# Kernel optimization log

Measured on AMD Instinct MI355X. Metric: run time of the kernel, lower is better.

## Reference

```python
import jax, jax.numpy as jnp
import numpy as np

B, N, E, H = 4, 8192, 256, 8
EXP = 4  # params['num_layers'] -> MLP expansion
HID = EXP * E
EPS = 1e-5


def _layernorm(x, w, b):
    mu = jnp.mean(x, axis=-1, keepdims=True)
    var = jnp.mean(jnp.square(x - mu), axis=-1, keepdims=True)
    return (x - mu) * jax.lax.rsqrt(var + EPS) * w + b


def _mish(x):
    return x * jnp.tanh(jax.nn.softplus(x))


def setup_inputs() -> dict:
    key = jax.random.key(0)
    ks = jax.random.split(key, 12)
    s = 0.02
    return {
        "x": jax.random.normal(ks[0], (B, N, E), dtype=jnp.float32),
        "ln1_w": jnp.ones((E,), jnp.float32),
        "ln1_b": jnp.zeros((E,), jnp.float32),
        "Wq": jax.random.normal(ks[1], (E, E), jnp.float32) * s,
        "bq": jnp.zeros((E,), jnp.float32),
        "Wk": jax.random.normal(ks[2], (E, E), jnp.float32) * s,
        "bk": jnp.zeros((E,), jnp.float32),
        "Wv": jax.random.normal(ks[3], (E, E), jnp.float32) * s,
        "bv": jnp.zeros((E,), jnp.float32),
        "Wp": jax.random.normal(ks[4], (E, E), jnp.float32) * s,
        "bp": jnp.zeros((E,), jnp.float32),
        "ln2_w": jnp.ones((E,), jnp.float32),
        "ln2_b": jnp.zeros((E,), jnp.float32),
        "W1": jax.random.normal(ks[5], (HID, E), jnp.float32) * s,
        "b1": jnp.zeros((HID,), jnp.float32),
        "W2": jax.random.normal(ks[6], (E, HID), jnp.float32) * s,
        "b2": jnp.zeros((E,), jnp.float32),
    }


def _msa(x, Wq, bq, Wk, bk, Wv, bv, Wp, bp):
    b, n, e = x.shape
    d = n // H  # sequence-chunk per head (faithful to source rearrange)
    q = (x @ Wq.T + bq).reshape(b, H, d, e)
    k = (x @ Wk.T + bk).reshape(b, H, d, e)
    v = (x @ Wv.T + bv).reshape(b, H, d, e)
    scale = jnp.sqrt(jnp.float32(E))
    energy = jnp.einsum('bhie,bhke->bhik', q, k)  # (b,H,d,d)
    att = jax.nn.softmax(energy, axis=3) / scale
    o = jnp.einsum('bhik,bhke->bhie', att, v).reshape(b, n, e)
    return o @ Wp.T + bp


def reference(x, ln1_w, ln1_b, Wq, bq, Wk, bk, Wv, bv, Wp, bp,
              ln2_w, ln2_b, W1, b1, W2, b2):
    # pre-LN attention block + residual
    x1 = _msa(_layernorm(x, ln1_w, ln1_b), Wq, bq, Wk, bk, Wv, bv, Wp, bp) + x
    # pre-LN MLP (Mish after both linears, per source) + residual
    h = _layernorm(x1, ln2_w, ln2_b)
    h = _mish(h @ W1.T + b1)
    h = _mish(h @ W2.T + b2)
    return h + x1
```

## Files before the change

kernel.cpp:

```cpp
#include <hip/hip_runtime.h>

typedef float  f32x4  __attribute__((ext_vector_type(4)));
typedef float  f4v    __attribute__((ext_vector_type(4)));
typedef __bf16 bf16x8 __attribute__((ext_vector_type(8)));
typedef __bf16 bf16x4 __attribute__((ext_vector_type(4)));
typedef unsigned short ushort_t;

#define AS1 __attribute__((address_space(1)))
#define AS3 __attribute__((address_space(3)))

static __device__ __forceinline__ void gload_lds16(const void* g, void* l) {
  __builtin_amdgcn_global_load_lds((const AS1 void*)g, (AS3 void*)l, 16, 0, 0);
}

static __device__ __forceinline__ float mishf(float x) {
  float t = __expf(x);
  float u = t * (t + 2.f);
  float y = x * __fdividef(u, u + 2.f);
  return (x > 15.f) ? x : y;
}

__global__ __launch_bounds__(256) void castw(
    const float* __restrict__ Wq, const float* __restrict__ Wk,
    const float* __restrict__ Wv, const float* __restrict__ Wp,
    const float* __restrict__ W1, const float* __restrict__ W2,
    __bf16* __restrict__ out)
{
  const int i = (blockIdx.x * 256 + threadIdx.x) * 4;
  const float* src; int off = i;
  if      (i < 65536)  { src = Wq; }
  else if (i < 131072) { src = Wk; off = i - 65536; }
  else if (i < 196608) { src = Wv; off = i - 131072; }
  else if (i < 262144) { src = Wp; off = i - 196608; }
  else if (i < 524288) { src = W1; off = i - 262144; }
  else                 { src = W2; off = i - 524288; }
  const f4v v = *(const f4v*)(src + off);
  bf16x4 o;
  #pragma unroll
  for (int j = 0; j < 4; ++j) o[j] = (__bf16)v[j];
  *(bf16x4*)(out + i) = o;
}

__global__ void packb(const float* __restrict__ a, const float* __restrict__ b,
                      const float* __restrict__ c, float* __restrict__ o) {
  int i = threadIdx.x;
  o[i] = (i < 256) ? a[i] : (i < 512 ? b[i - 256] : c[i - 512]);
}

__global__ __launch_bounds__(256) void ln_rows(
    const float* __restrict__ X, const float* __restrict__ g,
    const float* __restrict__ b, __bf16* __restrict__ Y)
{
  const int l = threadIdx.x & 63;
  const size_t row = (size_t)blockIdx.x * 4 + (threadIdx.x >> 6);
  const f4v x = *(const f4v*)(X + row * 256 + l * 4);
  float s = x[0] + x[1] + x[2] + x[3];
  float q = x[0]*x[0] + x[1]*x[1] + x[2]*x[2] + x[3]*x[3];
  #pragma unroll
  for (int d = 1; d < 64; d <<= 1) { s += __shfl_xor(s, d); q += __shfl_xor(q, d); }
  const float mu = s * (1.f / 256.f);
  const float rs = rsqrtf(q * (1.f / 256.f) - mu * mu + 1e-5f);
  const f4v gv = *(const f4v*)(g + l * 4);
  const f4v bv = *(const f4v*)(b + l * 4);
  bf16x4 o;
  #pragma unroll
  for (int j = 0; j < 4; ++j) o[j] = (__bf16)((x[j] - mu) * rs * gv[j] + bv[j]);
  *(bf16x4*)(Y + row * 256 + l * 4) = o;
}

template<int NT, int KC, int ACT, int RES, int OUTBF>
__global__ __launch_bounds__(512, 2) void bgemm(
    const __bf16* __restrict__ A, const __bf16* __restrict__ Wg,
    const float* __restrict__ bias, const float* __restrict__ res,
    void* __restrict__ out, int ldo)
{
  constexpr int K  = KC * 256;
  constexpr int NB = (KC > 1) ? 2 : 1;
  __shared__ __bf16 Ab[NB][128 * 256];
  const int tid = threadIdx.x, l = tid & 63, w = tid >> 6;
  constexpr int nwg = NT * 256;
  const int wg = (blockIdx.x & 7) * (nwg / 8) + (blockIdx.x >> 3);
  const int mt = wg / NT, nt = wg % NT;
  const int row0 = mt * 128;
  const int col0 = nt * 256 + w * 32;

  auto stageA = [&](int b, int c) {
    #pragma unroll
    for (int j = 0; j < 8; ++j) {
      const int s = j * 512 + tid;
      const int r = s >> 5, q = s & 31;
      gload_lds16(A + (size_t)(row0 + r) * K + c * 256 + ((q ^ (r & 7)) << 3),
                  &Ab[b][s << 3]);
    }
  };

  bf16x8 bf[2][8];
  auto loadB = [&](int c) {
    #pragma unroll
    for (int n = 0; n < 2; ++n)
      #pragma unroll
      for (int u = 0; u < 8; ++u)
        bf[n][u] = *(const bf16x8*)(Wg + (size_t)(col0 + n * 16 + (l & 15)) * K
                                      + c * 256 + u * 32 + ((l >> 4) << 3));
  };

  f32x4 acc[8][2] = {};

  loadB(0);
  stageA(0, 0);
  asm volatile("s_waitcnt vmcnt(0)" ::: "memory");
  __builtin_amdgcn_s_barrier();

  for (int c = 0; c < KC; ++c) {
    const __bf16* La = Ab[c & (NB - 1)];
    if (KC > 1 && c + 1 < KC) stageA((c + 1) & (NB - 1), c + 1);
    #pragma unroll
    for (int u = 0; u < 8; ++u) {
      bf16x8 af[8];
      #pragma unroll
      for (int m = 0; m < 8; ++m) {
        const int r = m * 16 + (l & 15);
        const int q = ((u << 2) | (l >> 4)) ^ (r & 7);
        af[m] = *(const bf16x8*)&La[((r << 5) | q) << 3];
      }
      #pragma unroll
      for (int m = 0; m < 8; ++m) {
        acc[m][0] = __builtin_amdgcn_mfma_f32_16x16x32_bf16(af[m], bf[0][u], acc[m][0], 0, 0, 0);
        acc[m][1] = __builtin_amdgcn_mfma_f32_16x16x32_bf16(af[m], bf[1][u], acc[m][1], 0, 0, 0);
      }
    }
    if (KC > 1 && c + 1 < KC) {
      loadB(c + 1);
      __syncthreads();
    }
  }

  const float b0 = bias[col0 + (l & 15)];
  const float b1 = bias[col0 + 16 + (l & 15)];
  #pragma unroll
  for (int m = 0; m < 8; ++m) {
    #pragma unroll
    for (int r = 0; r < 4; ++r) {
      const int row = row0 + m * 16 + ((l >> 4) << 2) + r;
      float v0 = acc[m][0][r] + b0;
      float v1 = acc[m][1][r] + b1;
      if (ACT) { v0 = mishf(v0); v1 = mishf(v1); }
      if (OUTBF) {
        __bf16* op = (__bf16*)out + (size_t)row * ldo + col0;
        op[l & 15]        = (__bf16)v0;
        op[16 + (l & 15)] = (__bf16)v1;
      } else {
        if (RES) {
          const float* rp = res + (size_t)row * ldo + col0;
          v0 += rp[l & 15];
          v1 += rp[16 + (l & 15)];
        }
        float* op = (float*)out + (size_t)row * ldo + col0;
        op[l & 15]        = v0;
        op[16 + (l & 15)] = v1;
      }
    }
  }
}

__global__ __launch_bounds__(512) void attn_fwd(
    const __bf16* __restrict__ QKV, __bf16* __restrict__ Om)
{
  __shared__ __bf16 Ks[2][32][256];
  __shared__ __bf16 Vs[2][256][32];
  __shared__ __bf16 Ps[8][16][32];
  const int tid = threadIdx.x, l = tid & 63, w = tid >> 6;
  const int wgs = (blockIdx.x & 7) * 32 + (blockIdx.x >> 3);
  const int bh = wgs >> 3, qt = wgs & 7;
  const size_t rbase = (size_t)bh * 1024 * 768;
  const int qr0 = qt * 128 + w * 16;

  bf16x8 qf[8];
  {
    const __bf16* qp = QKV + rbase + (size_t)(qr0 + (l & 15)) * 768 + ((l >> 4) << 3);
    #pragma unroll
    for (int s = 0; s < 8; ++s) qf[s] = *(const bf16x8*)(qp + s * 32);
  }
  f32x4 acc[16] = {};
  float lacc[4] = {0.f, 0.f, 0.f, 0.f};

  const int kec = tid & 31, kr_ = tid >> 5;
  const int vp = tid & 15, vc = tid >> 4;
  const __bf16* gK = QKV + 256 + rbase + kec * 8;
  const __bf16* gV = QKV + 512 + rbase + vc * 8;

  uint4 rk0, rk1, rv0, rv1;
  auto ldKV = [&](int kt) {
    const __bf16* k0 = gK + (size_t)(kt * 32 + kr_) * 768;
    rk0 = *(const uint4*)k0;
    rk1 = *(const uint4*)(k0 + 16 * 768);
    const __bf16* v0 = gV + (size_t)(kt * 32 + vp * 2) * 768;
    rv0 = *(const uint4*)v0;
    rv1 = *(const uint4*)(v0 + 768);
  };
  auto wrKV = [&](int buf) {
    char* kb = (char*)&Ks[buf][0][0];
    const int a0 = (kr_ * 512 + kec * 16) ^ ((kr_ & 15) << 4);
    const int a1 = ((kr_ + 16) * 512 + kec * 16) ^ (((kr_ + 16) & 15) << 4);
    *(uint4*)(kb + a0) = rk0;
    *(uint4*)(kb + a1) = rk1;
    const ushort_t* s0 = (const ushort_t*)&rv0;
    const ushort_t* s1 = (const ushort_t*)&rv1;
    #pragma unroll
    for (int i = 0; i < 8; ++i) {
      unsigned pk = (unsigned)s0[i] | ((unsigned)s1[i] << 16);
      *(unsigned*)&Vs[buf][vc * 8 + i][vp * 2] = pk;
    }
  };

  ldKV(0); wrKV(0);
  __syncthreads();
  int cur = 0;
  for (int kt = 0;;) {
    if (kt + 1 < 32) ldKV(kt + 1);
    f32x4 S[2] = {};
    const char* kbase = (const char*)&Ks[cur][0][0];
    #pragma unroll
    for (int t = 0; t < 2; ++t) {
      const int kcol = t * 16 + (l & 15);
      const int swz = (kcol & 15) << 4;
      #pragma unroll
      for (int s = 0; s < 8; ++s) {
        uint4 kf = *(const uint4*)(kbase + ((kcol * 512 + s * 64 + ((l >> 4) << 4)) ^ swz));
        S[t] = __builtin_amdgcn_mfma_f32_16x16x32_bf16(qf[s], __builtin_bit_cast(bf16x8, kf), S[t], 0, 0, 0);
      }
    }
    #pragma unroll
    for (int t = 0; t < 2; ++t)
      #pragma unroll
      for (int r = 0; r < 4; ++r) {
        float p = __expf(S[t][r]);
        lacc[r] += p;
        Ps[w][((l >> 4) << 2) + r][t * 16 + (l & 15)] = (__bf16)p;
      }
    bf16x8 pf = *(const bf16x8*)&Ps[w][l & 15][(l >> 4) << 3];
    #pragma unroll
    for (int n = 0; n < 16; ++n) {
      uint4 vf = *(const uint4*)&Vs[cur][n * 16 + (l & 15)][(l >> 4) << 3];
      acc[n] = __builtin_amdgcn_mfma_f32_16x16x32_bf16(pf, __builtin_bit_cast(bf16x8, vf), acc[n], 0, 0, 0);
    }
    if (++kt == 32) break;
    wrKV(cur ^ 1);
    __syncthreads();
    cur ^= 1;
  }
  f32x4 inv;
  #pragma unroll
  for (int r = 0; r < 4; ++r) {
    float s = lacc[r];
    s += __shfl_xor(s, 1); s += __shfl_xor(s, 2);
    s += __shfl_xor(s, 4); s += __shfl_xor(s, 8);
    inv[r] = 1.f / (16.f * s);
  }
  __bf16* op = Om + (size_t)(bh * 1024 + qr0 + ((l >> 4) << 2)) * 256 + (l & 15);
  #pragma unroll
  for (int n = 0; n < 16; ++n)
    #pragma unroll
    for (int r = 0; r < 4; ++r)
      op[(size_t)r * 256 + n * 16] = (__bf16)(acc[n][r] * inv[r]);
}

extern "C" void kernel_launch(void* const* d_in, const int* in_sizes, int n_in,
                              void* d_out, int out_size, void* d_ws, size_t ws_size,
                              hipStream_t stream)
{
  const float* x    = (const float*)d_in[0];
  const float* ln1w = (const float*)d_in[1];
  const float* ln1b = (const float*)d_in[2];
  const float* Wq   = (const float*)d_in[3];
  const float* bq   = (const float*)d_in[4];
  const float* Wk   = (const float*)d_in[5];
  const float* bk   = (const float*)d_in[6];
  const float* Wv   = (const float*)d_in[7];
  const float* bv   = (const float*)d_in[8];
  const float* Wp   = (const float*)d_in[9];
  const float* bp   = (const float*)d_in[10];
  const float* ln2w = (const float*)d_in[11];
  const float* ln2b = (const float*)d_in[12];
  const float* W1   = (const float*)d_in[13];
  const float* b1   = (const float*)d_in[14];
  const float* W2   = (const float*)d_in[15];
  const float* b2   = (const float*)d_in[16];

  char* ws = (char*)d_ws;
  __bf16* wb   = (__bf16*)(ws);
  float*  bqkv = (float*)(ws + 1572864);
  __bf16* y    = (__bf16*)(ws + 2097152);
  __bf16* qkv  = (__bf16*)(ws + 18874368);
  float*  x1   = (float*)(ws + 18874368);
  __bf16* hb   = (__bf16*)(ws + 52428800);
  __bf16* h1   = (__bf16*)(ws + 69206016);
  __bf16* ao   = y;
  float*  outp = (float*)d_out;

  castw<<<768, 256, 0, stream>>>(Wq, Wk, Wv, Wp, W1, W2, wb);
  packb<<<1, 768, 0, stream>>>(bq, bk, bv, bqkv);
  ln_rows<<<8192, 256, 0, stream>>>(x, ln1w, ln1b, y);
  bgemm<3, 1, 0, 0, 1><<<768,  512, 0, stream>>>(y,  wb,          bqkv, nullptr, qkv,  768);
  attn_fwd<<<256, 512, 0, stream>>>(qkv, ao);
  bgemm<1, 1, 0, 1, 0><<<256,  512, 0, stream>>>(ao, wb + 196608, bp,   x,       x1,   256);
  ln_rows<<<8192, 256, 0, stream>>>(x1, ln2w, ln2b, hb);
  bgemm<4, 1, 1, 0, 1><<<1024, 512, 0, stream>>>(hb, wb + 262144, b1,   nullptr, h1,  1024);
  bgemm<1, 4, 1, 1, 0><<<256,  512, 0, stream>>>(h1, wb + 524288, b2,   x1,      outp, 256);
}
```

Before: 236.5 us.

## Shrink attention blocks to 256 threads and single-buffer the GEMM A tile

The attention kernel now runs 512 blocks of 256 threads, each handling 64 query rows instead of 128. Each thread loads more K/V per tile, and the V and P shared arrays are padded to 34 columns to avoid bank conflicts. The GEMM drops its double-buffered A tile for a single buffer that is synchronously reloaded per K chunk. This halves LDS use, which should allow more resident blocks, at the cost of no longer overlapping loads with MFMA compute in the K=1024 GEMM.

```diff
diff --git a/kernel.cpp b/kernel.cpp
--- a/kernel.cpp
+++ b/kernel.cpp
@@ -74,9 +74,8 @@
     const float* __restrict__ bias, const float* __restrict__ res,
     void* __restrict__ out, int ldo)
 {
-  constexpr int K  = KC * 256;
-  constexpr int NB = (KC > 1) ? 2 : 1;
-  __shared__ __bf16 Ab[NB][128 * 256];
+  constexpr int K = KC * 256;
+  __shared__ __bf16 Ab[128 * 256];
   const int tid = threadIdx.x, l = tid & 63, w = tid >> 6;
   constexpr int nwg = NT * 256;
   const int wg = (blockIdx.x & 7) * (nwg / 8) + (blockIdx.x >> 3);
@@ -84,13 +83,13 @@
   const int row0 = mt * 128;
   const int col0 = nt * 256 + w * 32;
 
-  auto stageA = [&](int b, int c) {
+  auto stageA = [&](int c) {
     #pragma unroll
     for (int j = 0; j < 8; ++j) {
       const int s = j * 512 + tid;
       const int r = s >> 5, q = s & 31;
       gload_lds16(A + (size_t)(row0 + r) * K + c * 256 + ((q ^ (r & 7)) << 3),
-                  &Ab[b][s << 3]);
+                  &Ab[s << 3]);
     }
   };
 
@@ -106,14 +105,11 @@
 
   f32x4 acc[8][2] = {};
 
-  loadB(0);
-  stageA(0, 0);
+  stageA(0); loadB(0);
   asm volatile("s_waitcnt vmcnt(0)" ::: "memory");
   __builtin_amdgcn_s_barrier();
 
-  for (int c = 0; c < KC; ++c) {
-    const __bf16* La = Ab[c & (NB - 1)];
-    if (KC > 1 && c + 1 < KC) stageA((c + 1) & (NB - 1), c + 1);
+  for (int c = 0;;) {
     #pragma unroll
     for (int u = 0; u < 8; ++u) {
       bf16x8 af[8];
@@ -121,7 +117,7 @@
       for (int m = 0; m < 8; ++m) {
         const int r = m * 16 + (l & 15);
         const int q = ((u << 2) | (l >> 4)) ^ (r & 7);
-        af[m] = *(const bf16x8*)&La[((r << 5) | q) << 3];
+        af[m] = *(const bf16x8*)&Ab[((r << 5) | q) << 3];
       }
       #pragma unroll
       for (int m = 0; m < 8; ++m) {
@@ -129,10 +125,12 @@
         acc[m][1] = __builtin_amdgcn_mfma_f32_16x16x32_bf16(af[m], bf[1][u], acc[m][1], 0, 0, 0);
       }
     }
-    if (KC > 1 && c + 1 < KC) {
-      loadB(c + 1);
-      __syncthreads();
-    }
+    if (++c == KC) break;
+    __syncthreads();
+    stageA(c);
+    loadB(c);
+    asm volatile("s_waitcnt vmcnt(0)" ::: "memory");
+    __builtin_amdgcn_s_barrier();
   }
 
   const float b0 = bias[col0 + (l & 15)];
@@ -163,17 +161,17 @@
   }
 }
 
-__global__ __launch_bounds__(512) void attn_fwd(
+__global__ __launch_bounds__(256) void attn_fwd(
     const __bf16* __restrict__ QKV, __bf16* __restrict__ Om)
 {
   __shared__ __bf16 Ks[2][32][256];
-  __shared__ __bf16 Vs[2][256][32];
-  __shared__ __bf16 Ps[8][16][32];
+  __shared__ __bf16 Vs[2][256][34];
+  __shared__ __bf16 Ps[4][16][34];
   const int tid = threadIdx.x, l = tid & 63, w = tid >> 6;
-  const int wgs = (blockIdx.x & 7) * 32 + (blockIdx.x >> 3);
-  const int bh = wgs >> 3, qt = wgs & 7;
+  const int wgs = (blockIdx.x & 7) * 64 + (blockIdx.x >> 3);
+  const int bh = wgs >> 4, qt = wgs & 15;
   const size_t rbase = (size_t)bh * 1024 * 768;
-  const int qr0 = qt * 128 + w * 16;
+  const int qr0 = qt * 64 + w * 16;
 
   bf16x8 qf[8];
   {
@@ -185,31 +183,39 @@
   float lacc[4] = {0.f, 0.f, 0.f, 0.f};
 
   const int kec = tid & 31, kr_ = tid >> 5;
-  const int vp = tid & 15, vc = tid >> 4;
+  const int vp = tid & 15, vc0 = tid >> 4;
   const __bf16* gK = QKV + 256 + rbase + kec * 8;
-  const __bf16* gV = QKV + 512 + rbase + vc * 8;
-
-  uint4 rk0, rk1, rv0, rv1;
+  const __bf16* gV = QKV + 512 + rbase + vc0 * 8;
+
+  uint4 rk[4], rv[2][2];
   auto ldKV = [&](int kt) {
-    const __bf16* k0 = gK + (size_t)(kt * 32 + kr_) * 768;
-    rk0 = *(const uint4*)k0;
-    rk1 = *(const uint4*)(k0 + 16 * 768);
-    const __bf16* v0 = gV + (size_t)(kt * 32 + vp * 2) * 768;
-    rv0 = *(const uint4*)v0;
-    rv1 = *(const uint4*)(v0 + 768);
+    #pragma unroll
+    for (int j = 0; j < 4; ++j)
+      rk[j] = *(const uint4*)(gK + (size_t)(kt * 32 + kr_ + 8 * j) * 768);
+    #pragma unroll
+    for (int h = 0; h < 2; ++h) {
+      const __bf16* v0 = gV + h * 128 + (size_t)(kt * 32 + vp * 2) * 768;
+      rv[h][0] = *(const uint4*)v0;
+      rv[h][1] = *(const uint4*)(v0 + 768);
+    }
   };
   auto wrKV = [&](int buf) {
     char* kb = (char*)&Ks[buf][0][0];
-    const int a0 = (kr_ * 512 + kec * 16) ^ ((kr_ & 15) << 4);
-    const int a1 = ((kr_ + 16) * 512 + kec * 16) ^ (((kr_ + 16) & 15) << 4);
-    *(uint4*)(kb + a0) = rk0;
-    *(uint4*)(kb + a1) = rk1;
-    const ushort_t* s0 = (const ushort_t*)&rv0;
-    const ushort_t* s1 = (const ushort_t*)&rv1;
-    #pragma unroll
-    for (int i = 0; i < 8; ++i) {
-      unsigned pk = (unsigned)s0[i] | ((unsigned)s1[i] << 16);
-      *(unsigned*)&Vs[buf][vc * 8 + i][vp * 2] = pk;
+    #pragma unroll
+    for (int j = 0; j < 4; ++j) {
+      const int r = kr_ + 8 * j;
+      *(uint4*)(kb + ((r * 512 + kec * 16) ^ ((r & 15) << 4))) = rk[j];
+    }
+    #pragma unroll
+    for (int h = 0; h < 2; ++h) {
+      const int vcc = vc0 + 16 * h;
+      const ushort_t* s0 = (const ushort_t*)&rv[h][0];
+      const ushort_t* s1 = (const ushort_t*)&rv[h][1];
+      #pragma unroll
+      for (int i = 0; i < 8; ++i) {
+        unsigned pk = (unsigned)s0[i] | ((unsigned)s1[i] << 16);
+        *(unsigned*)&Vs[buf][vcc * 8 + i][vp * 2] = pk;
+      }
     }
   };
 
@@ -302,7 +308,7 @@
   packb<<<1, 768, 0, stream>>>(bq, bk, bv, bqkv);
   ln_rows<<<8192, 256, 0, stream>>>(x, ln1w, ln1b, y);
   bgemm<3, 1, 0, 0, 1><<<768,  512, 0, stream>>>(y,  wb,          bqkv, nullptr, qkv,  768);
-  attn_fwd<<<256, 512, 0, stream>>>(qkv, ao);
+  attn_fwd<<<512, 256, 0, stream>>>(qkv, ao);
   bgemm<1, 1, 0, 1, 0><<<256,  512, 0, stream>>>(ao, wb + 196608, bp,   x,       x1,   256);
   ln_rows<<<8192, 256, 0, stream>>>(x1, ln2w, ln2b, hb);
   bgemm<4, 1, 1, 0, 1><<<1024, 512, 0, stream>>>(hb, wb + 262144, b1,   nullptr, h1,  1024);
```

Measured after the change: 289.8 us. 1.23x slower.
